# Performance work log

Hardware: AMD Instinct MI355X
Metric: run time of the kernel (lower is better)

Reference implementation:

```python
import jax, jax.numpy as jnp
import numpy as np

BETA = 0.25
N, D, K = 131072, 128, 1024  # points, embed dim, codebook size


def setup_inputs() -> dict:
    key = jax.random.key(0)
    k1, k2 = jax.random.split(key)
    x = jax.random.normal(k1, (N, D), dtype=jnp.float32)
    emb = jax.random.normal(k2, (K, D), dtype=jnp.float32)  # codebook (nn.Embedding weight)
    return {"x": x, "emb": emb}


def reference(x, emb):
    dist = (jnp.sum(x * x, axis=1, keepdims=True)
            + jnp.sum(emb * emb, axis=1)
            - 2.0 * (x @ emb.T))
    index = jnp.argmin(dist, axis=1)          # [N]
    # one_hot @ emb == gather of nearest code
    quantized = emb[index]                    # [N, D]
    commitment_loss = jnp.mean((jax.lax.stop_gradient(quantized) - x) ** 2)
    embedding_loss = jnp.mean((quantized - jax.lax.stop_gradient(x)) ** 2)
    vq_loss = commitment_loss * BETA + embedding_loss
    # straight-through estimator
    quantized_st = x + jax.lax.stop_gradient(quantized - x)
    return index[:, None], quantized_st, vq_loss
```

## Files before the change

kernel.cpp:

```cpp
#include <hip/hip_runtime.h>

#define NPTS 131072
#define DIM  128
#define KC   1024
#define CHB  16640

using half8 = __attribute__((ext_vector_type(8))) _Float16;
using f32x4 = __attribute__((ext_vector_type(4))) float;

static __device__ __forceinline__ unsigned umax_(unsigned a, unsigned b){ return a > b ? a : b; }
static __device__ __forceinline__ unsigned med3u(unsigned a, unsigned b, unsigned c){
    unsigned d;
    asm("v_med3_u32 %0, %1, %2, %3" : "=v"(d) : "v"(a), "v"(b), "v"(c));
    return d;
}


__global__ void vq_prep(const float* __restrict__ emb, unsigned short* __restrict__ wsE,
                        float* __restrict__ eeW) {
    int lane = threadIdx.x & 63, wv = threadIdx.x >> 6;
    int code = blockIdx.x * 4 + wv;
    const float* e = emb + (size_t)code * DIM;
    float a = e[lane], b = e[lane + 64];

    int chunk = code >> 6, r = code & 63, swz = (r & 7) << 4;
    size_t base = (size_t)chunk * 16384 + (size_t)(r << 8);
    _Float16 ha = (_Float16)a, hb = (_Float16)b;
    wsE[(base + (size_t)(((lane << 1))        ^ swz)) >> 1] = __builtin_bit_cast(unsigned short, ha);
    wsE[(base + (size_t)(((lane + 64) << 1)   ^ swz)) >> 1] = __builtin_bit_cast(unsigned short, hb);

    float v = a * a + b * b;
    #pragma unroll
    for (int o = 32; o > 0; o >>= 1) v += __shfl_down(v, o);
    if (lane == 0) eeW[code] = 0.5f * v - 512.0f;
}

__global__ __launch_bounds__(256, 4) void vq_mfma(const float* __restrict__ x,
                                                  const float* __restrict__ emb,
                                                  const unsigned short* __restrict__ wsE,
                                                  const float* __restrict__ eeW,
                                                  float* __restrict__ out,
                                                  float* __restrict__ bsum) {
    __shared__ __attribute__((aligned(128))) char lds[2][CHB];
    const int tid  = threadIdx.x;
    const int lane = tid & 63, wv = tid >> 6;
    const int g    = lane >> 4, c = lane & 15;
    const int blockbase = blockIdx.x * 128;

    half8 ah[2][4];
    #pragma unroll
    for (int rt = 0; rt < 2; ++rt) {
        const float* xr = x + (size_t)(blockbase + wv * 32 + rt * 16 + c) * DIM;
        #pragma unroll
        for (int kc = 0; kc < 4; ++kc) {
            const float4* p = reinterpret_cast<const float4*>(xr + kc * 32 + g * 8);
            float4 v0 = p[0], v1 = p[1];
            half8 hh;
            hh[0] = (_Float16)v0.x; hh[1] = (_Float16)v0.y;
            hh[2] = (_Float16)v0.z; hh[3] = (_Float16)v0.w;
            hh[4] = (_Float16)v1.x; hh[5] = (_Float16)v1.y;
            hh[6] = (_Float16)v1.z; hh[7] = (_Float16)v1.w;
            ah[rt][kc] = hh;
        }
    }

    unsigned m1[8], m2[8], m3[8];
    #pragma unroll
    for (int i = 0; i < 8; ++i) { m1[i] = 0u; m2[i] = 0u; m3[i] = 0u; }

    #define STAGE(BUF, CH)                                                                   \
        do {                                                                                 \
            const char* src_ = (const char*)wsE + (size_t)(CH) * 16384 + (size_t)wv * 4096;  \
            char* dst_ = &lds[(BUF)][0] + wv * 4096;                                         \
            _Pragma("unroll")                                                                \
            for (int it = 0; it < 4; ++it) {                                                 \
                __builtin_amdgcn_global_load_lds(                                            \
                    (const __attribute__((address_space(1))) void*)(src_ + it * 1024 + lane * 16), \
                    (__attribute__((address_space(3))) void*)(dst_ + it * 1024),             \
                    16, 0, 0);                                                               \
            }                                                                                \
            if (wv == 0) {                                                                   \
                __builtin_amdgcn_global_load_lds(                                            \
                    (const __attribute__((address_space(1))) void*)(eeW + (size_t)(CH) * 64 + lane), \
                    (__attribute__((address_space(3))) void*)(&lds[(BUF)][0] + 16384),       \
                    4, 0, 0);                                                                \
            }                                                                                \
        } while (0)

    STAGE(0, 0);
    __syncthreads();

    for (int ch = 0; ch < 16; ++ch) {
        if (ch < 15) STAGE((ch + 1) & 1, ch + 1);
        const char* L = &lds[ch & 1][0];

        #pragma unroll
        for (int ct = 0; ct < 4; ++ct) {
            const int r   = ct * 16 + c;
            const int swz = (r & 7) << 4;
            const float eec = *reinterpret_cast<const float*>(L + 16384 + (r << 2));
            f32x4 acc0 = {-eec, -eec, -eec, -eec};
            f32x4 acc1 = {-eec, -eec, -eec, -eec};
            #pragma unroll
            for (int kc = 0; kc < 4; ++kc) {
                int bo = (r << 8) + (((kc << 6) + (g << 4)) ^ swz);
                half8 bh = *reinterpret_cast<const half8*>(L + bo);
                acc0 = __builtin_amdgcn_mfma_f32_16x16x32_f16(ah[0][kc], bh, acc0, 0, 0, 0);
                acc1 = __builtin_amdgcn_mfma_f32_16x16x32_f16(ah[1][kc], bh, acc1, 0, 0, 0);
            }
            const unsigned codeC = (unsigned)(1023 - (ch * 64 + r));
            #pragma unroll
            for (int q = 0; q < 4; ++q) {
                #pragma unroll
                for (int rt = 0; rt < 2; ++rt) {
                    float sp = (rt ? acc1[q] : acc0[q]);
                    unsigned u   = __builtin_bit_cast(unsigned, sp);
                    unsigned key = (u & 0xFFFFFC00u) | codeC;
                    const int i = rt * 4 + q;
                    m3[i] = med3u(m2[i], m3[i], key);
                    m2[i] = med3u(m1[i], m2[i], key);
                    m1[i] = umax_(m1[i], key);
                }
            }
        }
        __syncthreads();
    }

    int* lbest = reinterpret_cast<int*>(&lds[0][0]);
    #pragma unroll
    for (int rt = 0; rt < 2; ++rt) {
        #pragma unroll
        for (int q = 0; q < 4; ++q) {
            const int i = rt * 4 + q;
            unsigned a1 = m1[i], a2 = m2[i], a3 = m3[i];
            #pragma unroll
            for (int mk = 1; mk < 16; mk <<= 1) {
                unsigned b1 = (unsigned)__shfl_xor((int)a1, mk, 64);
                unsigned b2 = (unsigned)__shfl_xor((int)a2, mk, 64);
                unsigned b3 = (unsigned)__shfl_xor((int)a3, mk, 64);
                unsigned c1 = umax_(a1, b1), t1 = (a1 < b1 ? a1 : b1);
                unsigned u1 = umax_(a2, b2), u2 = (a2 < b2 ? a2 : b2);
                unsigned c2 = umax_(t1, u1), t2 = (t1 < u1 ? t1 : u1);
                unsigned c3 = umax_(umax_(t2, u2), umax_(a3, b3));
                a1 = c1; a2 = c2; a3 = c3;
            }
            if (c == 0) {
                int lrow = wv * 32 + rt * 16 + g * 4 + q;
                int i1 = 1023 - (int)(a1 & 1023u);
                int i2 = 1023 - (int)(a2 & 1023u);
                int i3 = 1023 - (int)(a3 & 1023u);
                lbest[lrow] = i1 | (i2 << 10) | (i3 << 20);
            }
        }
    }
    __syncthreads();

    {
        const int lrow = tid >> 1, hf = tid & 1;
        const int grow = blockbase + lrow;
        const int pk = lbest[lrow];
        const int ia = pk & 1023, ib = (pk >> 10) & 1023, ic = (pk >> 20) & 1023;

        const float4* xv4 = reinterpret_cast<const float4*>(x + (size_t)grow * DIM + hf * 64);
        float4 xr[16];
        #pragma unroll
        for (int i = 0; i < 16; ++i) xr[i] = xv4[i];

        const float4* ea = reinterpret_cast<const float4*>(emb + (size_t)ia * DIM + hf * 64);
        const float4* eb = reinterpret_cast<const float4*>(emb + (size_t)ib * DIM + hf * 64);
        const float4* ec = reinterpret_cast<const float4*>(emb + (size_t)ic * DIM + hf * 64);
        float da = 0.f, db = 0.f, dc = 0.f;
        #pragma unroll
        for (int i = 0; i < 16; ++i) {
            float4 va = ea[i], vb = eb[i], vc = ec[i], xx = xr[i];
            float ax = va.x - xx.x, ay = va.y - xx.y, az = va.z - xx.z, aw = va.w - xx.w;
            float bx = vb.x - xx.x, by = vb.y - xx.y, bz = vb.z - xx.z, bw = vb.w - xx.w;
            float cx = vc.x - xx.x, cy = vc.y - xx.y, cz = vc.z - xx.z, cw = vc.w - xx.w;
            da += ax * ax + ay * ay + az * az + aw * aw;
            db += bx * bx + by * by + bz * bz + bw * bw;
            dc += cx * cx + cy * cy + cz * cz + cw * cw;
        }
        da += __shfl_xor(da, 1, 64);
        db += __shfl_xor(db, 1, 64);
        dc += __shfl_xor(dc, 1, 64);

        int idx = ia; float dm = da;
        if (db < dm || (db == dm && ib < idx)) { dm = db; idx = ib; }
        if (dc < dm || (dc == dm && ic < idx)) { dm = dc; idx = ic; }

        if (hf == 0) out[grow] = (float)idx;

        const float4* q4 = reinterpret_cast<const float4*>(emb + (size_t)idx * DIM + hf * 64);
        float4* oq = reinterpret_cast<float4*>(out + (size_t)NPTS + (size_t)grow * DIM + hf * 64);
        float lsum = 0.f;
        #pragma unroll
        for (int i = 0; i < 16; ++i) {
            float4 qv = q4[i];
            oq[i] = qv;
            float dx = qv.x - xr[i].x;
            float dy = qv.y - xr[i].y;
            float dz = qv.z - xr[i].z;
            float dw = qv.w - xr[i].w;
            lsum += dx * dx + dy * dy + dz * dz + dw * dw;
        }
        __shared__ float red[4];
        #pragma unroll
        for (int o = 32; o > 0; o >>= 1) lsum += __shfl_down(lsum, o);
        if (lane == 0) red[wv] = lsum;
        __syncthreads();
        if (tid == 0) bsum[blockIdx.x] = (red[0] + red[1]) + (red[2] + red[3]);
    }
    #undef STAGE
}

__global__ void vq_finalize(const float* __restrict__ bsum, float* __restrict__ out) {
    __shared__ float red[16];
    int t = threadIdx.x;
    float v = bsum[t];
    #pragma unroll
    for (int o = 32; o > 0; o >>= 1) v += __shfl_down(v, o);
    if ((t & 63) == 0) red[t >> 6] = v;
    __syncthreads();
    if (t == 0) {
        float s = 0.f;
        #pragma unroll
        for (int i = 0; i < 16; ++i) s += red[i];
        out[(size_t)NPTS + (size_t)NPTS * DIM] = 1.25f * s / 16777216.0f;
    }
}

__global__ void vq_ee(const float* __restrict__ emb, float* __restrict__ eeW) {
    int gid  = blockIdx.x * blockDim.x + threadIdx.x;
    int w    = gid >> 6;
    int lane = threadIdx.x & 63;
    const float* e = emb + (size_t)w * DIM;
    float a = e[lane];
    float b = e[lane + 64];
    float v = a * a + b * b;
    #pragma unroll
    for (int o = 32; o > 0; o >>= 1) v += __shfl_down(v, o);
    if (lane == 0) eeW[w] = 0.5f * v - 512.0f;
}

__global__ __launch_bounds__(256, 1) void vq_main(const float* __restrict__ x,
                                                  const float* __restrict__ emb,
                                                  const float* __restrict__ eeW,
                                                  float* __restrict__ out,
                                                  float* __restrict__ bsum) {
    const int p = blockIdx.x * 256 + threadIdx.x;
    float4 xr[32];
    const float4* xv = reinterpret_cast<const float4*>(x + (size_t)p * DIM);
    #pragma unroll
    for (int i = 0; i < 32; ++i) xr[i] = xv[i];
    float bestv = -3.4e38f; int bi = 0;
    for (int k = 0; k < KC; ++k) {
        const int ku = __builtin_amdgcn_readfirstlane(k);
        const float4* e4 = reinterpret_cast<const float4*>(emb + (size_t)ku * DIM);
        float a0 = 0.f, a1 = 0.f, a2 = 0.f, a3 = 0.f;
        #pragma unroll
        for (int i = 0; i < 32; ++i) {
            float4 ev = e4[i];
            a0 = fmaf(xr[i].x, ev.x, a0);
            a1 = fmaf(xr[i].y, ev.y, a1);
            a2 = fmaf(xr[i].z, ev.z, a2);
            a3 = fmaf(xr[i].w, ev.w, a3);
        }
        float s = ((a0 + a1) + (a2 + a3)) - eeW[ku];
        if (s > bestv) { bestv = s; bi = k; }
    }
    out[p] = (float)bi;
    const float4* q4 = reinterpret_cast<const float4*>(emb + (size_t)bi * DIM);
    float4* oq = reinterpret_cast<float4*>(out + (size_t)NPTS + (size_t)p * DIM);
    float lsum = 0.f;
    #pragma unroll
    for (int i = 0; i < 32; ++i) {
        float4 qv = q4[i];
        oq[i] = qv;
        float dx = qv.x - xr[i].x;
        float dy = qv.y - xr[i].y;
        float dz = qv.z - xr[i].z;
        float dw = qv.w - xr[i].w;
        lsum += dx * dx + dy * dy + dz * dz + dw * dw;
    }
    __shared__ float red[4];
    #pragma unroll
    for (int o = 32; o > 0; o >>= 1) lsum += __shfl_down(lsum, o);
    int lane = threadIdx.x & 63, wvl = threadIdx.x >> 6;
    if (lane == 0) red[wvl] = lsum;
    __syncthreads();
    if (threadIdx.x == 0) bsum[blockIdx.x] = (red[0] + red[1]) + (red[2] + red[3]);
}

__global__ void vq_finalize512(const float* __restrict__ bsum, float* __restrict__ out) {
    __shared__ float red[8];
    int t = threadIdx.x;
    float v = bsum[t];
    #pragma unroll
    for (int o = 32; o > 0; o >>= 1) v += __shfl_down(v, o);
    if ((t & 63) == 0) red[t >> 6] = v;
    __syncthreads();
    if (t == 0) {
        float s = 0.f;
        #pragma unroll
        for (int i = 0; i < 8; ++i) s += red[i];
        out[(size_t)NPTS + (size_t)NPTS * DIM] = 1.25f * s / 16777216.0f;
    }
}

extern "C" void kernel_launch(void* const* d_in, const int* in_sizes, int n_in,
                              void* d_out, int out_size, void* d_ws, size_t ws_size,
                              hipStream_t stream) {
    const float* x   = (const float*)d_in[0];
    const float* emb = (const float*)d_in[1];
    float* out = (float*)d_out;
    char*  ws  = (char*)d_ws;

    if (ws_size >= 270336) {
        unsigned short* wsE = (unsigned short*)ws;
        float* eeW  = (float*)(ws + 262144);
        float* bsum = (float*)(ws + 266240);
        vq_prep<<<256, 256, 0, stream>>>(emb, wsE, eeW);
        vq_mfma<<<1024, 256, 0, stream>>>(x, emb, wsE, eeW, out, bsum);
        vq_finalize<<<1, 1024, 0, stream>>>(bsum, out);
    } else {
        float* eeW  = (float*)ws;
        float* bsum = (float*)ws + 1024;
        vq_ee<<<256, 256, 0, stream>>>(emb, eeW);
        vq_main<<<512, 256, 0, stream>>>(x, emb, eeW, out, bsum);
        vq_finalize512<<<1, 512, 0, stream>>>(bsum, out);
    }
}
```

Baseline: 117.8 us.

## Software-pipeline LDS codebook loads, prefetch x early, reuse rerank distance for loss

```diff
diff --git a/kernel.cpp b/kernel.cpp
--- a/kernel.cpp
+++ b/kernel.cpp
@@ -87,8 +87,21 @@
             }                                                                                \
         } while (0)
 
+    #define PRELOAD(L_, CT_)                                                                 \
+        do {                                                                                 \
+            const int rp_  = (CT_) * 16 + c;                                                 \
+            const int swp_ = (rp_ & 7) << 4;                                                 \
+            _Pragma("unroll")                                                                \
+            for (int kc = 0; kc < 4; ++kc)                                                   \
+                bq[kc] = *reinterpret_cast<const half8*>((L_) + (rp_ << 8) + (((kc << 6) + (g << 4)) ^ swp_)); \
+            eecq = *reinterpret_cast<const float*>((L_) + 16384 + (rp_ << 2));               \
+        } while (0)
+
+    half8 bq[4]; float eecq;
+
     STAGE(0, 0);
     __syncthreads();
+    PRELOAD(&lds[0][0], 0);
 
     for (int ch = 0; ch < 16; ++ch) {
         if (ch < 15) STAGE((ch + 1) & 1, ch + 1);
@@ -96,19 +109,22 @@
 
         #pragma unroll
         for (int ct = 0; ct < 4; ++ct) {
-            const int r   = ct * 16 + c;
-            const int swz = (r & 7) << 4;
-            const float eec = *reinterpret_cast<const float*>(L + 16384 + (r << 2));
+            half8 b0 = bq[0], b1v = bq[1], b2v = bq[2], b3v = bq[3];
+            const float eec = eecq;
+            if (ct < 3) PRELOAD(L, ct + 1);
+
             f32x4 acc0 = {-eec, -eec, -eec, -eec};
             f32x4 acc1 = {-eec, -eec, -eec, -eec};
-            #pragma unroll
-            for (int kc = 0; kc < 4; ++kc) {
-                int bo = (r << 8) + (((kc << 6) + (g << 4)) ^ swz);
-                half8 bh = *reinterpret_cast<const half8*>(L + bo);
-                acc0 = __builtin_amdgcn_mfma_f32_16x16x32_f16(ah[0][kc], bh, acc0, 0, 0, 0);
-                acc1 = __builtin_amdgcn_mfma_f32_16x16x32_f16(ah[1][kc], bh, acc1, 0, 0, 0);
-            }
-            const unsigned codeC = (unsigned)(1023 - (ch * 64 + r));
+            acc0 = __builtin_amdgcn_mfma_f32_16x16x32_f16(ah[0][0], b0,  acc0, 0, 0, 0);
+            acc1 = __builtin_amdgcn_mfma_f32_16x16x32_f16(ah[1][0], b0,  acc1, 0, 0, 0);
+            acc0 = __builtin_amdgcn_mfma_f32_16x16x32_f16(ah[0][1], b1v, acc0, 0, 0, 0);
+            acc1 = __builtin_amdgcn_mfma_f32_16x16x32_f16(ah[1][1], b1v, acc1, 0, 0, 0);
+            acc0 = __builtin_amdgcn_mfma_f32_16x16x32_f16(ah[0][2], b2v, acc0, 0, 0, 0);
+            acc1 = __builtin_amdgcn_mfma_f32_16x16x32_f16(ah[1][2], b2v, acc1, 0, 0, 0);
+            acc0 = __builtin_amdgcn_mfma_f32_16x16x32_f16(ah[0][3], b3v, acc0, 0, 0, 0);
+            acc1 = __builtin_amdgcn_mfma_f32_16x16x32_f16(ah[1][3], b3v, acc1, 0, 0, 0);
+
+            const unsigned codeC = (unsigned)(1023 - (ch * 64 + ct * 16 + c));
             #pragma unroll
             for (int q = 0; q < 4; ++q) {
                 #pragma unroll
@@ -124,7 +140,15 @@
             }
         }
         __syncthreads();
-    }
+        if (ch < 15) PRELOAD(&lds[(ch + 1) & 1][0], 0);
+    }
+
+    const int lrow = tid >> 1, hf = tid & 1;
+    const int grow = blockbase + lrow;
+    const float4* xv4 = reinterpret_cast<const float4*>(x + (size_t)grow * DIM + hf * 64);
+    float4 xr[16];
+    #pragma unroll
+    for (int i = 0; i < 8; ++i) xr[i] = xv4[i];
 
     int* lbest = reinterpret_cast<int*>(&lds[0][0]);
     #pragma unroll
@@ -145,26 +169,22 @@
                 a1 = c1; a2 = c2; a3 = c3;
             }
             if (c == 0) {
-                int lrow = wv * 32 + rt * 16 + g * 4 + q;
+                int lr = wv * 32 + rt * 16 + g * 4 + q;
                 int i1 = 1023 - (int)(a1 & 1023u);
                 int i2 = 1023 - (int)(a2 & 1023u);
                 int i3 = 1023 - (int)(a3 & 1023u);
-                lbest[lrow] = i1 | (i2 << 10) | (i3 << 20);
+                lbest[lr] = i1 | (i2 << 10) | (i3 << 20);
             }
         }
     }
     __syncthreads();
 
+    #pragma unroll
+    for (int i = 8; i < 16; ++i) xr[i] = xv4[i];
+
     {
-        const int lrow = tid >> 1, hf = tid & 1;
-        const int grow = blockbase + lrow;
         const int pk = lbest[lrow];
         const int ia = pk & 1023, ib = (pk >> 10) & 1023, ic = (pk >> 20) & 1023;
-
-        const float4* xv4 = reinterpret_cast<const float4*>(x + (size_t)grow * DIM + hf * 64);
-        float4 xr[16];
-        #pragma unroll
-        for (int i = 0; i < 16; ++i) xr[i] = xv4[i];
 
         const float4* ea = reinterpret_cast<const float4*>(emb + (size_t)ia * DIM + hf * 64);
         const float4* eb = reinterpret_cast<const float4*>(emb + (size_t)ib * DIM + hf * 64);
@@ -192,17 +212,10 @@
 
         const float4* q4 = reinterpret_cast<const float4*>(emb + (size_t)idx * DIM + hf * 64);
         float4* oq = reinterpret_cast<float4*>(out + (size_t)NPTS + (size_t)grow * DIM + hf * 64);
-        float lsum = 0.f;
-        #pragma unroll
-        for (int i = 0; i < 16; ++i) {
-            float4 qv = q4[i];
-            oq[i] = qv;
-            float dx = qv.x - xr[i].x;
-            float dy = qv.y - xr[i].y;
-            float dz = qv.z - xr[i].z;
-            float dw = qv.w - xr[i].w;
-            lsum += dx * dx + dy * dy + dz * dz + dw * dw;
-        }
+        #pragma unroll
+        for (int i = 0; i < 16; ++i) oq[i] = q4[i];
+
+        float lsum = (hf == 0) ? dm : 0.f;
         __shared__ float red[4];
         #pragma unroll
         for (int o = 32; o > 0; o >>= 1) lsum += __shfl_down(lsum, o);
@@ -211,6 +224,7 @@
         if (tid == 0) bsum[blockIdx.x] = (red[0] + red[1]) + (red[2] + red[3]);
     }
     #undef STAGE
+    #undef PRELOAD
 }
 
 __global__ void vq_finalize(const float* __restrict__ bsum, float* __restrict__ out) {
```

After: 107.4 us. -8.8%, faster.
